# Kernel optimization log

Hardware: AMD Instinct MI355X
Metric: run time of the kernel (lower is better)

The kernel has to match this reference:

```python
import jax, jax.numpy as jnp
import numpy as np
import math

B, N = 512, 32
OBS, NA = 128, 16
OA = OBS + NA  # 144
DK = 64


def setup_inputs() -> dict:
    key = jax.random.key(0)
    ks = jax.random.split(key, 12)
    return {
        "states": jax.random.normal(ks[0], (B, N, OBS), jnp.float32),
        "policies": jax.random.uniform(ks[1], (B, N, NA), jnp.float32),
        "actions": jax.random.uniform(ks[2], (B, N, NA), jnp.float32),
        "W_obs": jax.random.normal(ks[3], (64, OBS), jnp.float32) * 0.05,
        "b_obs": jax.random.normal(ks[4], (64,), jnp.float32) * 0.05,
        "W_oa": jax.random.normal(ks[5], (64, OA), jnp.float32) * 0.05,
        "b_oa": jax.random.normal(ks[6], (64,), jnp.float32) * 0.05,
        "W_key": jax.random.normal(ks[7], (DK, 64), jnp.float32) * 0.05,
        "W_query": jax.random.normal(ks[8], (DK, 64), jnp.float32) * 0.05,
        "W_attn_val": jax.random.normal(ks[9], (64, 64), jnp.float32) * 0.05,
        "W_f1": jax.random.normal(ks[10], (64, 64), jnp.float32) * 0.05,
        "W_f2": jax.random.normal(ks[11], (16, 64), jnp.float32) * 0.05,
    }


def reference(states, policies, actions, W_obs, b_obs, W_oa, b_oa,
              W_key, W_query, W_attn_val, W_f1, W_f2):
    num_agents = states.shape[1]
    d_k = W_attn_val.shape[0]  # d_k_obs == obs_act_output_dim

    obs_actions = jnp.concatenate([states, actions], axis=-1)   # [B,N,OA]
    obs_policy = jnp.concatenate([states, policies], axis=-1)   # [B,N,OA]

    states_embed = jax.nn.relu(states @ W_obs.T + b_obs)        # [B,N,64]
    key_obs = states_embed @ W_key.T                            # [B,N,DK]
    query_obs = states_embed @ W_query.T                        # [B,N,DK]

    # score after transpose(1,2): score[b,j,i] = q_i . k_j ; softmax over i
    score = jnp.einsum('bid,bjd->bji', query_obs, key_obs)
    weight = jax.nn.softmax(score / math.sqrt(d_k), axis=-1)    # [B,N,N]

    # mixed input: for row j, entry i uses policy if i==j else action
    eye = jnp.eye(num_agents, dtype=states.dtype)[None, :, :, None]  # [1,N,N,1]
    oap = eye * obs_policy[:, None, :, :] + (1.0 - eye) * obs_actions[:, None, :, :]  # [B,N,N,OA]

    emb = jax.nn.relu(oap @ W_oa.T + b_oa)                      # [B,N,N,64]
    attn_vals = jnp.tanh(emb @ W_attn_val.T)                    # [B,N,N,64]

    node_features = jnp.mean(attn_vals * weight[..., None], axis=2)  # [B,N,64]

    value = jax.nn.leaky_relu(node_features @ W_f1.T)           # slope 0.01, matches torch default
    value = value @ W_f2.T                                      # [B,N,16]
    return value, weight
```

## Files before the change

### kernel.cpp

```cpp
#include <hip/hip_runtime.h>

typedef _Float16 f16;
typedef _Float16 f16x8 __attribute__((ext_vector_type(8)));
typedef float f32x4 __attribute__((ext_vector_type(4)));

#define MFMA16(a, b, c) __builtin_amdgcn_mfma_f32_16x16x32_f16((a), (b), (c), 0, 0, 0)

#define XS_HI  0
#define XS_LO  4352
#define E_HI   8704
#define E_LO   11008
#define EA_HI  13312
#define EA_LO  15616
#define EP_HI  17920
#define EP_LO  20224
#define KB_HI  22528
#define KB_LO  24832
#define QB_HI  27136
#define QB_LO  29440
#define AAT_HI 31744
#define AAT_LO 34304
#define WM_HI  36864
#define WM_LO  38144
#define WDIAG  39424
#define SMTOT  39488

__device__ __forceinline__ void split1(float v, ushort& h, ushort& lo) {
    f16 hf = (f16)v;
    float r = v - (float)hf;
    f16 lf = (f16)r;
    union { f16 f; ushort u; } a, b;
    a.f = hf; b.f = lf;
    h = a.u; lo = b.u;
}
__device__ __forceinline__ void split4(f32x4 v, ushort4& h, ushort4& l) {
    split1(v[0], h.x, l.x);
    split1(v[1], h.y, l.y);
    split1(v[2], h.z, l.z);
    split1(v[3], h.w, l.w);
}
__device__ __forceinline__ void mk8(float4 a, float4 b, f16x8& hi, f16x8& lo) {
    float v[8] = {a.x, a.y, a.z, a.w, b.x, b.y, b.z, b.w};
    #pragma unroll
    for (int j = 0; j < 8; ++j) {
        f16 h = (f16)v[j];
        hi[j] = h;
        lo[j] = (f16)(v[j] - (float)h);
    }
}
__device__ __forceinline__ void ldraw(const float* p, f16x8& h, f16x8& l) {
    float4 a = *(const float4*)p;
    float4 b = *(const float4*)(p + 4);
    mk8(a, b, h, l);
}
__device__ __forceinline__ f16x8 ldf(const ushort* sm, int off) {
    return *(const f16x8*)(sm + off);
}
__device__ __forceinline__ float fast_tanh(float x) {
    float xc = fminf(fmaxf(x, -9.0f), 9.0f);
    float e = __expf(2.0f * xc);
    return (e - 1.0f) * __builtin_amdgcn_rcpf(e + 1.0f);
}

__global__ void __launch_bounds__(256, 2)
critic_mfma(const float* __restrict__ states, const float* __restrict__ policies,
            const float* __restrict__ actions, const float* __restrict__ b_obs,
            const float* __restrict__ b_oa,
            const float* __restrict__ W_obs, const float* __restrict__ W_oa,
            const float* __restrict__ W_key, const float* __restrict__ W_query,
            const float* __restrict__ W_av,  const float* __restrict__ W_f1,
            const float* __restrict__ W_f2,
            float* __restrict__ out_value,
            float* __restrict__ out_weight)
{
    __shared__ ushort sm[SMTOT];
    const int b = blockIdx.x;
    const int t = threadIdx.x;
    const int wv = t >> 6, l = t & 63;
    const int lr = l & 15;
    const int lg = l >> 4;
    const int ft = wv;
    const int row = ft * 16 + lr;
    const int f0 = ft * 16 + lg * 4;

    float4 sv[4];
    {
        const float4* src = (const float4*)(states + (size_t)b * 4096);
        #pragma unroll
        for (int r4 = 0; r4 < 4; ++r4) sv[r4] = src[t + r4 * 256];
    }

    f16x8 wObsH[4], wObsL[4], wOaH[4], wOaL[4];
    #pragma unroll
    for (int c = 0; c < 4; ++c) {
        ldraw(W_obs + row * 128 + c * 32 + lg * 8, wObsH[c], wObsL[c]);
        ldraw(W_oa + row * 144 + c * 32 + lg * 8, wOaH[c], wOaL[c]);
    }
    f16x8 wTailH, wTailL;
    {
        float4 t0 = make_float4(0.f, 0.f, 0.f, 0.f), t1 = t0;
        if (lg < 2) {
            t0 = *(const float4*)(W_oa + row * 144 + 128 + lg * 8);
            t1 = *(const float4*)(W_oa + row * 144 + 132 + lg * 8);
        }
        mk8(t0, t1, wTailH, wTailL);
    }

    f16x8 actH[2], actL[2], polH[2], polL[2];
    #pragma unroll
    for (int at = 0; at < 2; ++at) {
        float4 a0v = make_float4(0.f, 0.f, 0.f, 0.f), a1v = a0v, p0v = a0v, p1v = a0v;
        if (lg < 2) {
            size_t base = (size_t)b * 512 + (at * 16 + lr) * 16 + lg * 8;
            a0v = *(const float4*)(actions + base);
            a1v = *(const float4*)(actions + base + 4);
            p0v = *(const float4*)(policies + base);
            p1v = *(const float4*)(policies + base + 4);
        }
        mk8(a0v, a1v, actH[at], actL[at]);
        mk8(p0v, p1v, polH[at], polL[at]);
    }

    #pragma unroll
    for (int r4 = 0; r4 < 4; ++r4) {
        int e4 = t + r4 * 256, srow = e4 >> 5, k0 = (e4 & 31) * 4;
        ushort4 h, lo;
        split1(sv[r4].x, h.x, lo.x);
        split1(sv[r4].y, h.y, lo.y);
        split1(sv[r4].z, h.z, lo.z);
        split1(sv[r4].w, h.w, lo.w);
        *(ushort4*)(sm + XS_HI + srow * 136 + k0) = h;
        *(ushort4*)(sm + XS_LO + srow * 136 + k0) = lo;
    }
    __syncthreads();

    const f32x4 Z = {0.f, 0.f, 0.f, 0.f};

    f32x4 accE[2] = {Z, Z}, accP[2] = {Z, Z};
    #pragma unroll
    for (int c = 0; c < 4; ++c) {
        #pragma unroll
        for (int at = 0; at < 2; ++at) {
            int ao = (at * 16 + lr) * 136 + c * 32 + lg * 8;
            f16x8 xh = ldf(sm, XS_HI + ao), xl = ldf(sm, XS_LO + ao);
            accE[at] = MFMA16(wObsH[c], xh, accE[at]);
            accE[at] = MFMA16(wObsH[c], xl, accE[at]);
            accE[at] = MFMA16(wObsL[c], xh, accE[at]);
            accP[at] = MFMA16(wOaH[c], xh, accP[at]);
            accP[at] = MFMA16(wOaH[c], xl, accP[at]);
            accP[at] = MFMA16(wOaL[c], xh, accP[at]);
        }
    }
    f32x4 accEA[2], accEP[2];
    #pragma unroll
    for (int at = 0; at < 2; ++at) {
        accEA[at] = accP[at]; accEP[at] = accP[at];
        accEA[at] = MFMA16(wTailH, actH[at], accEA[at]);
        accEA[at] = MFMA16(wTailH, actL[at], accEA[at]);
        accEA[at] = MFMA16(wTailL, actH[at], accEA[at]);
        accEP[at] = MFMA16(wTailH, polH[at], accEP[at]);
        accEP[at] = MFMA16(wTailH, polL[at], accEP[at]);
        accEP[at] = MFMA16(wTailL, polH[at], accEP[at]);
    }

    f16x8 wKH[2], wKL[2], wQH[2], wQL[2], wVH[2], wVL[2];
    #pragma unroll
    for (int c = 0; c < 2; ++c) {
        ldraw(W_key + row * 64 + c * 32 + lg * 8, wKH[c], wKL[c]);
        ldraw(W_query + row * 64 + c * 32 + lg * 8, wQH[c], wQL[c]);
        ldraw(W_av + row * 64 + c * 32 + lg * 8, wVH[c], wVL[c]);
    }

    {
        float4 bo = *(const float4*)&b_obs[f0];
        float4 ba = *(const float4*)&b_oa[f0];
        #pragma unroll
        for (int at = 0; at < 2; ++at) {
            int agent = at * 16 + lr;
            f32x4 e, ea, ep;
            e[0] = fmaxf(accE[at][0] + bo.x, 0.f);  e[1] = fmaxf(accE[at][1] + bo.y, 0.f);
            e[2] = fmaxf(accE[at][2] + bo.z, 0.f);  e[3] = fmaxf(accE[at][3] + bo.w, 0.f);
            ea[0] = fmaxf(accEA[at][0] + ba.x, 0.f); ea[1] = fmaxf(accEA[at][1] + ba.y, 0.f);
            ea[2] = fmaxf(accEA[at][2] + ba.z, 0.f); ea[3] = fmaxf(accEA[at][3] + ba.w, 0.f);
            ep[0] = fmaxf(accEP[at][0] + ba.x, 0.f); ep[1] = fmaxf(accEP[at][1] + ba.y, 0.f);
            ep[2] = fmaxf(accEP[at][2] + ba.z, 0.f); ep[3] = fmaxf(accEP[at][3] + ba.w, 0.f);
            ushort4 h, lo;
            split4(e, h, lo);
            *(ushort4*)(sm + E_HI + agent * 72 + f0) = h;
            *(ushort4*)(sm + E_LO + agent * 72 + f0) = lo;
            split4(ea, h, lo);
            *(ushort4*)(sm + EA_HI + agent * 72 + f0) = h;
            *(ushort4*)(sm + EA_LO + agent * 72 + f0) = lo;
            split4(ep, h, lo);
            *(ushort4*)(sm + EP_HI + agent * 72 + f0) = h;
            *(ushort4*)(sm + EP_LO + agent * 72 + f0) = lo;
        }
    }
    __syncthreads();

    f32x4 dDiff[2];
    {
        f32x4 aK[2] = {Z, Z}, aQ[2] = {Z, Z}, aA[2] = {Z, Z}, aP[2] = {Z, Z};
        #pragma unroll
        for (int c = 0; c < 2; ++c) {
            #pragma unroll
            for (int at = 0; at < 2; ++at) {
                int ao = (at * 16 + lr) * 72 + c * 32 + lg * 8;
                f16x8 eh = ldf(sm, E_HI + ao),  el = ldf(sm, E_LO + ao);
                f16x8 xh = ldf(sm, EA_HI + ao), xl = ldf(sm, EA_LO + ao);
                f16x8 yh = ldf(sm, EP_HI + ao), yl = ldf(sm, EP_LO + ao);
                aK[at] = MFMA16(wKH[c], eh, aK[at]);
                aK[at] = MFMA16(wKH[c], el, aK[at]);
                aK[at] = MFMA16(wKL[c], eh, aK[at]);
                aQ[at] = MFMA16(wQH[c], eh, aQ[at]);
                aQ[at] = MFMA16(wQH[c], el, aQ[at]);
                aQ[at] = MFMA16(wQL[c], eh, aQ[at]);
                aA[at] = MFMA16(wVH[c], xh, aA[at]);
                aA[at] = MFMA16(wVH[c], xl, aA[at]);
                aA[at] = MFMA16(wVL[c], xh, aA[at]);
                aP[at] = MFMA16(wVH[c], yh, aP[at]);
                aP[at] = MFMA16(wVH[c], yl, aP[at]);
                aP[at] = MFMA16(wVL[c], yh, aP[at]);
            }
        }
        #pragma unroll
        for (int at = 0; at < 2; ++at) {
            int agent = at * 16 + lr;
            ushort4 h, lo;
            split4(aK[at], h, lo);
            *(ushort4*)(sm + KB_HI + agent * 72 + f0) = h;
            *(ushort4*)(sm + KB_LO + agent * 72 + f0) = lo;
            split4(aQ[at], h, lo);
            *(ushort4*)(sm + QB_HI + agent * 72 + f0) = h;
            *(ushort4*)(sm + QB_LO + agent * 72 + f0) = lo;
            f32x4 ta, tp;
            #pragma unroll
            for (int r = 0; r < 4; ++r) {
                ta[r] = fast_tanh(aA[at][r]);
                tp[r] = fast_tanh(aP[at][r]);
            }
            dDiff[at] = tp - ta;
            #pragma unroll
            for (int r = 0; r < 4; ++r) {
                ushort hh, ll;
                split1(ta[r], hh, ll);
                sm[AAT_HI + (f0 + r) * 40 + agent] = hh;
                sm[AAT_LO + (f0 + r) * 40 + agent] = ll;
            }
        }
    }

    f16x8 wF1H[2], wF1L[2], wF2H[2], wF2L[2];
    #pragma unroll
    for (int c = 0; c < 2; ++c)
        ldraw(W_f1 + row * 64 + c * 32 + lg * 8, wF1H[c], wF1L[c]);
    if (wv < 2) {
        #pragma unroll
        for (int c = 0; c < 2; ++c)
            ldraw(W_f2 + lr * 64 + c * 32 + lg * 8, wF2H[c], wF2L[c]);
    }
    __syncthreads();

    if (wv < 2) {
        int jt = wv;
        f16x8 kh[2], kl[2];
        #pragma unroll
        for (int c = 0; c < 2; ++c) {
            int ko = (jt * 16 + lr) * 72 + c * 32 + lg * 8;
            kh[c] = ldf(sm, KB_HI + ko);
            kl[c] = ldf(sm, KB_LO + ko);
        }
        f32x4 s[2] = {Z, Z};
        #pragma unroll
        for (int c = 0; c < 2; ++c) {
            #pragma unroll
            for (int it = 0; it < 2; ++it) {
                int qo = (it * 16 + lr) * 72 + c * 32 + lg * 8;
                f16x8 qh = ldf(sm, QB_HI + qo), ql = ldf(sm, QB_LO + qo);
                s[it] = MFMA16(kh[c], qh, s[it]);
                s[it] = MFMA16(kh[c], ql, s[it]);
                s[it] = MFMA16(kl[c], qh, s[it]);
            }
        }
        float* wdiag = (float*)(sm + WDIAG);
        #pragma unroll
        for (int r = 0; r < 4; ++r) {
            int j = jt * 16 + lg * 4 + r;
            float v0 = s[0][r] * 0.125f, v1 = s[1][r] * 0.125f;
            float m = fmaxf(v0, v1);
            #pragma unroll
            for (int off = 1; off < 16; off <<= 1)
                m = fmaxf(m, __shfl_xor(m, off, 16));
            float e0 = __expf(v0 - m), e1 = __expf(v1 - m);
            float su = e0 + e1;
            #pragma unroll
            for (int off = 1; off < 16; off <<= 1)
                su += __shfl_xor(su, off, 16);
            float inv = 1.0f / su;
            e0 *= inv; e1 *= inv;
            out_weight[(size_t)b * 1024 + j * 32 + lr] = e0;
            out_weight[(size_t)b * 1024 + j * 32 + 16 + lr] = e1;
            ushort hh, ll;
            split1(e0, hh, ll);
            sm[WM_HI + j * 40 + lr] = hh;
            sm[WM_LO + j * 40 + lr] = ll;
            split1(e1, hh, ll);
            sm[WM_HI + j * 40 + 16 + lr] = hh;
            sm[WM_LO + j * 40 + 16 + lr] = ll;
            if (lr == lg * 4 + r) wdiag[j] = jt ? e1 : e0;
        }
    }
    __syncthreads();

    {
        int fo = (ft * 16 + lr) * 40 + lg * 8;
        f16x8 ah = ldf(sm, AAT_HI + fo);
        f16x8 al = ldf(sm, AAT_LO + fo);
        const float* wdiag = (const float*)(sm + WDIAG);
        #pragma unroll
        for (int jt = 0; jt < 2; ++jt) {
            int j = jt * 16 + lr;
            f16x8 wh = ldf(sm, WM_HI + j * 40 + lg * 8);
            f16x8 wl = ldf(sm, WM_LO + j * 40 + lg * 8);
            f32x4 acc = Z;
            acc = MFMA16(ah, wh, acc);
            acc = MFMA16(ah, wl, acc);
            acc = MFMA16(al, wh, acc);
            float wd = wdiag[j];
            f32x4 nf;
            #pragma unroll
            for (int r = 0; r < 4; ++r)
                nf[r] = (acc[r] + wd * dDiff[jt][r]) * 0.03125f;
            ushort4 h, lo;
            split4(nf, h, lo);
            *(ushort4*)(sm + E_HI + j * 72 + f0) = h;
            *(ushort4*)(sm + E_LO + j * 72 + f0) = lo;
        }
    }
    __syncthreads();

    {
        f32x4 hA[2] = {Z, Z};
        #pragma unroll
        for (int c = 0; c < 2; ++c) {
            #pragma unroll
            for (int jt = 0; jt < 2; ++jt) {
                int bo2 = (jt * 16 + lr) * 72 + c * 32 + lg * 8;
                f16x8 nh_ = ldf(sm, E_HI + bo2), nl_ = ldf(sm, E_LO + bo2);
                hA[jt] = MFMA16(wF1H[c], nh_, hA[jt]);
                hA[jt] = MFMA16(wF1H[c], nl_, hA[jt]);
                hA[jt] = MFMA16(wF1L[c], nh_, hA[jt]);
            }
        }
        #pragma unroll
        for (int jt = 0; jt < 2; ++jt) {
            int j = jt * 16 + lr;
            f32x4 hv;
            #pragma unroll
            for (int r = 0; r < 4; ++r)
                hv[r] = fmaxf(hA[jt][r], 0.01f * hA[jt][r]);
            ushort4 h, lo;
            split4(hv, h, lo);
            *(ushort4*)(sm + EA_HI + j * 72 + f0) = h;
            *(ushort4*)(sm + EA_LO + j * 72 + f0) = lo;
        }
    }
    __syncthreads();

    if (wv < 2) {
        int jt = wv;
        f32x4 acc = Z;
        #pragma unroll
        for (int c = 0; c < 2; ++c) {
            int ho = (jt * 16 + lr) * 72 + c * 32 + lg * 8;
            f16x8 hh = ldf(sm, EA_HI + ho), hl = ldf(sm, EA_LO + ho);
            acc = MFMA16(wF2H[c], hh, acc);
            acc = MFMA16(wF2H[c], hl, acc);
            acc = MFMA16(wF2L[c], hh, acc);
        }
        int j = jt * 16 + lr;
        *(float4*)&out_value[(size_t)b * 512 + j * 16 + lg * 4] =
            make_float4(acc[0], acc[1], acc[2], acc[3]);
    }
}

extern "C" void kernel_launch(void* const* d_in, const int* in_sizes, int n_in,
                              void* d_out, int out_size, void* d_ws, size_t ws_size,
                              hipStream_t stream) {
    const float* states   = (const float*)d_in[0];
    const float* policies = (const float*)d_in[1];
    const float* actions  = (const float*)d_in[2];
    const float* W_obs    = (const float*)d_in[3];
    const float* b_obs    = (const float*)d_in[4];
    const float* W_oa     = (const float*)d_in[5];
    const float* b_oa     = (const float*)d_in[6];
    const float* W_key    = (const float*)d_in[7];
    const float* W_query  = (const float*)d_in[8];
    const float* W_av     = (const float*)d_in[9];
    const float* W_f1     = (const float*)d_in[10];
    const float* W_f2     = (const float*)d_in[11];

    float* out_value  = (float*)d_out;
    float* out_weight = (float*)d_out + 512 * 32 * 16;

    critic_mfma<<<512, 256, 0, stream>>>(states, policies, actions, b_obs, b_oa,
                                         W_obs, W_oa, W_key, W_query, W_av, W_f1, W_f2,
                                         out_value, out_weight);
}
```

Baseline: 19.28 us.

## Reassociate W_f1 into attention values and load states directly to registers

Applies W_f1 to the tanh attention values and the diagonal difference before the weighted-mean product, so the f1 GEMM runs on waves 2-3 while waves 0-1 compute scores and softmax. This removes one barrier-separated stage from the critical path. States are now loaded and split into fp16 hi/lo fragments straight into registers, which drops the LDS staging round trip and a barrier. The price is more register pressure and a second GEMM on the diagonal-difference term.

```diff
diff --git a/kernel.cpp b/kernel.cpp
--- a/kernel.cpp
+++ b/kernel.cpp
@@ -6,24 +6,27 @@
 
 #define MFMA16(a, b, c) __builtin_amdgcn_mfma_f32_16x16x32_f16((a), (b), (c), 0, 0, 0)
 
-#define XS_HI  0
-#define XS_LO  4352
-#define E_HI   8704
-#define E_LO   11008
-#define EA_HI  13312
-#define EA_LO  15616
-#define EP_HI  17920
-#define EP_LO  20224
-#define KB_HI  22528
-#define KB_LO  24832
-#define QB_HI  27136
-#define QB_LO  29440
-#define AAT_HI 31744
-#define AAT_LO 34304
-#define WM_HI  36864
-#define WM_LO  38144
-#define WDIAG  39424
-#define SMTOT  39488
+#define E_HI   0
+#define E_LO   2304
+#define GT_HI  0
+#define GT_LO  2304
+#define EA_HI  4608
+#define EA_LO  6912
+#define EP_HI  9216
+#define EP_LO  11520
+#define G2F_O  9216
+#define KB_HI  13824
+#define KB_LO  16128
+#define QB_HI  18432
+#define QB_LO  20736
+#define AAN_HI 23040
+#define AAN_LO 25344
+#define DDN_HI 27648
+#define DDN_LO 29952
+#define WM_HI  32256
+#define WM_LO  33536
+#define WDIAG  34816
+#define SMTOT  34880
 
 __device__ __forceinline__ void split1(float v, ushort& h, ushort& lo) {
     f16 hf = (f16)v;
@@ -83,12 +86,13 @@
     const int row = ft * 16 + lr;
     const int f0 = ft * 16 + lg * 4;
 
-    float4 sv[4];
-    {
-        const float4* src = (const float4*)(states + (size_t)b * 4096);
-        #pragma unroll
-        for (int r4 = 0; r4 < 4; ++r4) sv[r4] = src[t + r4 * 256];
-    }
+    f16x8 sxh[2][4], sxl[2][4];
+    #pragma unroll
+    for (int at = 0; at < 2; ++at)
+        #pragma unroll
+        for (int c = 0; c < 4; ++c)
+            ldraw(states + (size_t)b * 4096 + (at * 16 + lr) * 128 + c * 32 + lg * 8,
+                  sxh[at][c], sxl[at][c]);
 
     f16x8 wObsH[4], wObsL[4], wOaH[4], wOaL[4];
     #pragma unroll
@@ -121,19 +125,6 @@
         mk8(p0v, p1v, polH[at], polL[at]);
     }
 
-    #pragma unroll
-    for (int r4 = 0; r4 < 4; ++r4) {
-        int e4 = t + r4 * 256, srow = e4 >> 5, k0 = (e4 & 31) * 4;
-        ushort4 h, lo;
-        split1(sv[r4].x, h.x, lo.x);
-        split1(sv[r4].y, h.y, lo.y);
-        split1(sv[r4].z, h.z, lo.z);
-        split1(sv[r4].w, h.w, lo.w);
-        *(ushort4*)(sm + XS_HI + srow * 136 + k0) = h;
-        *(ushort4*)(sm + XS_LO + srow * 136 + k0) = lo;
-    }
-    __syncthreads();
-
     const f32x4 Z = {0.f, 0.f, 0.f, 0.f};
 
     f32x4 accE[2] = {Z, Z}, accP[2] = {Z, Z};
@@ -141,14 +132,12 @@
     for (int c = 0; c < 4; ++c) {
         #pragma unroll
         for (int at = 0; at < 2; ++at) {
-            int ao = (at * 16 + lr) * 136 + c * 32 + lg * 8;
-            f16x8 xh = ldf(sm, XS_HI + ao), xl = ldf(sm, XS_LO + ao);
-            accE[at] = MFMA16(wObsH[c], xh, accE[at]);
-            accE[at] = MFMA16(wObsH[c], xl, accE[at]);
-            accE[at] = MFMA16(wObsL[c], xh, accE[at]);
-            accP[at] = MFMA16(wOaH[c], xh, accP[at]);
-            accP[at] = MFMA16(wOaH[c], xl, accP[at]);
-            accP[at] = MFMA16(wOaL[c], xh, accP[at]);
+            accE[at] = MFMA16(wObsH[c], sxh[at][c], accE[at]);
+            accE[at] = MFMA16(wObsH[c], sxl[at][c], accE[at]);
+            accE[at] = MFMA16(wObsL[c], sxh[at][c], accE[at]);
+            accP[at] = MFMA16(wOaH[c], sxh[at][c], accP[at]);
+            accP[at] = MFMA16(wOaH[c], sxl[at][c], accP[at]);
+            accP[at] = MFMA16(wOaL[c], sxh[at][c], accP[at]);
         }
     }
     f32x4 accEA[2], accEP[2];
@@ -198,7 +187,6 @@
     }
     __syncthreads();
 
-    f32x4 dDiff[2];
     {
         f32x4 aK[2] = {Z, Z}, aQ[2] = {Z, Z}, aA[2] = {Z, Z}, aP[2] = {Z, Z};
         #pragma unroll
@@ -233,31 +221,37 @@
             split4(aQ[at], h, lo);
             *(ushort4*)(sm + QB_HI + agent * 72 + f0) = h;
             *(ushort4*)(sm + QB_LO + agent * 72 + f0) = lo;
-            f32x4 ta, tp;
+            f32x4 ta, tp, dd;
             #pragma unroll
             for (int r = 0; r < 4; ++r) {
                 ta[r] = fast_tanh(aA[at][r]);
                 tp[r] = fast_tanh(aP[at][r]);
+                dd[r] = tp[r] - ta[r];
             }
-            dDiff[at] = tp - ta;
-            #pragma unroll
-            for (int r = 0; r < 4; ++r) {
-                ushort hh, ll;
-                split1(ta[r], hh, ll);
-                sm[AAT_HI + (f0 + r) * 40 + agent] = hh;
-                sm[AAT_LO + (f0 + r) * 40 + agent] = ll;
-            }
-        }
-    }
-
-    f16x8 wF1H[2], wF1L[2], wF2H[2], wF2L[2];
-    #pragma unroll
-    for (int c = 0; c < 2; ++c)
-        ldraw(W_f1 + row * 64 + c * 32 + lg * 8, wF1H[c], wF1L[c]);
+            split4(ta, h, lo);
+            *(ushort4*)(sm + AAN_HI + agent * 72 + f0) = h;
+            *(ushort4*)(sm + AAN_LO + agent * 72 + f0) = lo;
+            split4(dd, h, lo);
+            *(ushort4*)(sm + DDN_HI + agent * 72 + f0) = h;
+            *(ushort4*)(sm + DDN_LO + agent * 72 + f0) = lo;
+        }
+    }
+
+    f16x8 wF2H[2], wF2L[2];
+    f16x8 wG1H[2][2], wG1L[2][2];
     if (wv < 2) {
         #pragma unroll
         for (int c = 0; c < 2; ++c)
             ldraw(W_f2 + lr * 64 + c * 32 + lg * 8, wF2H[c], wF2L[c]);
+    } else {
+        int w = wv - 2;
+        #pragma unroll
+        for (int gi = 0; gi < 2; ++gi) {
+            int gft = w * 2 + gi;
+            #pragma unroll
+            for (int c = 0; c < 2; ++c)
+                ldraw(W_f1 + (gft * 16 + lr) * 64 + c * 32 + lg * 8, wG1H[gi][c], wG1L[gi][c]);
+        }
     }
     __syncthreads();
 
@@ -309,56 +303,67 @@
             sm[WM_LO + j * 40 + 16 + lr] = ll;
             if (lr == lg * 4 + r) wdiag[j] = jt ? e1 : e0;
         }
+    } else {
+        int w = wv - 2;
+        float* G2Ff = (float*)(sm + G2F_O);
+        #pragma unroll
+        for (int gi = 0; gi < 2; ++gi) {
+            int gft = w * 2 + gi;
+            #pragma unroll
+            for (int it = 0; it < 2; ++it) {
+                f32x4 aG = Z, aG2 = Z;
+                #pragma unroll
+                for (int c = 0; c < 2; ++c) {
+                    int ao = (it * 16 + lr) * 72 + c * 32 + lg * 8;
+                    f16x8 anh = ldf(sm, AAN_HI + ao), anl = ldf(sm, AAN_LO + ao);
+                    f16x8 ddh = ldf(sm, DDN_HI + ao), ddl = ldf(sm, DDN_LO + ao);
+                    aG  = MFMA16(wG1H[gi][c], anh, aG);
+                    aG  = MFMA16(wG1H[gi][c], anl, aG);
+                    aG  = MFMA16(wG1L[gi][c], anh, aG);
+                    aG2 = MFMA16(wG1H[gi][c], ddh, aG2);
+                    aG2 = MFMA16(wG1H[gi][c], ddl, aG2);
+                    aG2 = MFMA16(wG1L[gi][c], ddh, aG2);
+                }
+                #pragma unroll
+                for (int r = 0; r < 4; ++r) {
+                    int f = gft * 16 + lg * 4 + r;
+                    int i = it * 16 + lr;
+                    ushort hh, ll;
+                    split1(aG[r], hh, ll);
+                    sm[GT_HI + f * 36 + i] = hh;
+                    sm[GT_LO + f * 36 + i] = ll;
+                    G2Ff[i * 68 + f] = aG2[r];
+                }
+            }
+        }
     }
     __syncthreads();
 
     {
-        int fo = (ft * 16 + lr) * 40 + lg * 8;
-        f16x8 ah = ldf(sm, AAT_HI + fo);
-        f16x8 al = ldf(sm, AAT_LO + fo);
+        int fo = (ft * 16 + lr) * 36 + lg * 8;
+        f16x8 gh = ldf(sm, GT_HI + fo);
+        f16x8 gl = ldf(sm, GT_LO + fo);
         const float* wdiag = (const float*)(sm + WDIAG);
+        const float* G2Ff = (const float*)(sm + G2F_O);
         #pragma unroll
         for (int jt = 0; jt < 2; ++jt) {
             int j = jt * 16 + lr;
             f16x8 wh = ldf(sm, WM_HI + j * 40 + lg * 8);
             f16x8 wl = ldf(sm, WM_LO + j * 40 + lg * 8);
             f32x4 acc = Z;
-            acc = MFMA16(ah, wh, acc);
-            acc = MFMA16(ah, wl, acc);
-            acc = MFMA16(al, wh, acc);
+            acc = MFMA16(gh, wh, acc);
+            acc = MFMA16(gh, wl, acc);
+            acc = MFMA16(gl, wh, acc);
             float wd = wdiag[j];
-            f32x4 nf;
+            float4 g2v = *(const float4*)(G2Ff + j * 68 + f0);
+            f32x4 hv;
+            hv[0] = (acc[0] + wd * g2v.x) * 0.03125f;
+            hv[1] = (acc[1] + wd * g2v.y) * 0.03125f;
+            hv[2] = (acc[2] + wd * g2v.z) * 0.03125f;
+            hv[3] = (acc[3] + wd * g2v.w) * 0.03125f;
             #pragma unroll
             for (int r = 0; r < 4; ++r)
-                nf[r] = (acc[r] + wd * dDiff[jt][r]) * 0.03125f;
-            ushort4 h, lo;
-            split4(nf, h, lo);
-            *(ushort4*)(sm + E_HI + j * 72 + f0) = h;
-            *(ushort4*)(sm + E_LO + j * 72 + f0) = lo;
-        }
-    }
-    __syncthreads();
-
-    {
-        f32x4 hA[2] = {Z, Z};
-        #pragma unroll
-        for (int c = 0; c < 2; ++c) {
-            #pragma unroll
-            for (int jt = 0; jt < 2; ++jt) {
-                int bo2 = (jt * 16 + lr) * 72 + c * 32 + lg * 8;
-                f16x8 nh_ = ldf(sm, E_HI + bo2), nl_ = ldf(sm, E_LO + bo2);
-                hA[jt] = MFMA16(wF1H[c], nh_, hA[jt]);
-                hA[jt] = MFMA16(wF1H[c], nl_, hA[jt]);
-                hA[jt] = MFMA16(wF1L[c], nh_, hA[jt]);
-            }
-        }
-        #pragma unroll
-        for (int jt = 0; jt < 2; ++jt) {
-            int j = jt * 16 + lr;
-            f32x4 hv;
-            #pragma unroll
-            for (int r = 0; r < 4; ++r)
-                hv[r] = fmaxf(hA[jt][r], 0.01f * hA[jt][r]);
+                hv[r] = fmaxf(hv[r], 0.01f * hv[r]);
             ushort4 h, lo;
             split4(hv, h, lo);
             *(ushort4*)(sm + EA_HI + j * 72 + f0) = h;
```

Result: slower. 23.47 us (+21.7%).
